# Optimization experiments

Hardware: AMD Instinct MI355X
Metric: run time of the kernel (lower is better)

The kernel has to match this reference:

```python
import jax, jax.numpy as jnp
import numpy as np

B, IN_DIM = 1024, 128
MBD_IN, MBD_OUT, MBD_K = 64, 50, 5
BN_EPS = 1e-5


def setup_inputs() -> dict:
    key = jax.random.key(0)
    ks = jax.random.split(key, 16)
    n = lambda k, s: jax.random.normal(k, s, dtype=jnp.float32)
    return {
        "x": n(ks[0], (B, IN_DIM)),
        # MLP: 128->256->128(BN)->64, LeakyReLU(0.2)
        "W1": n(ks[1], (IN_DIM, 256)) * 0.05, "b1": jnp.zeros((256,), jnp.float32),
        "W2": n(ks[2], (256, 128)) * 0.05, "b2": jnp.zeros((128,), jnp.float32),
        "gamma": jnp.ones((128,), jnp.float32), "beta": jnp.zeros((128,), jnp.float32),
        "W3": n(ks[3], (128, 64)) * 0.05, "b3": jnp.zeros((64,), jnp.float32),
        # SelfAttention1D(64, heads=1) on a length-1 token: softmax over a single
        # key is identically 1, so output = residual + out_proj(value_proj(h)).
        # Wq/Wk provably do not affect the output and are omitted.
        "Wv": n(ks[4], (64, 64)) * 0.05, "bv": jnp.zeros((64,), jnp.float32),
        "Wo": n(ks[5], (64, 64)) * 0.05, "bo": jnp.zeros((64,), jnp.float32),
        # MinibatchDiscrimination tensor T: [64, 50, 5], init 0.05*randn as in source
        "T": n(ks[6], (MBD_IN, MBD_OUT, MBD_K)) * 0.05,
        "Ws": n(ks[7], (MBD_IN + MBD_OUT, 1)) * 0.05, "bs": jnp.zeros((1,), jnp.float32),
    }


def _lrelu(h):
    return jnp.where(h > 0, h, 0.2 * h)


def reference(x, W1, b1, W2, b2, gamma, beta, W3, b3, Wv, bv, Wo, bo, T, Ws, bs):
    # --- MLP backbone (BatchNorm1d in training mode: batch statistics) ---
    h = _lrelu(x @ W1 + b1)                      # [B,256]
    h = h @ W2 + b2                              # [B,128]
    mu = h.mean(axis=0)
    var = ((h - mu) ** 2).mean(axis=0)           # biased variance (torch BN)
    h = (h - mu) * jax.lax.rsqrt(var + BN_EPS) * gamma + beta
    h = _lrelu(h)
    h = _lrelu(h @ W3 + b3)                      # [B,64]
    # --- SelfAttention1D, seq_len=1 -> attn weights == 1 ---
    h = h + (h @ Wv + bv) @ Wo + bo              # [B,64]
    # --- Minibatch discrimination: fused all-pairs L1 + exp-sum ---
    M = (h @ T.reshape(MBD_IN, MBD_OUT * MBD_K)).reshape(-1, MBD_OUT, MBD_K)  # [B,50,5]
    diff = jnp.abs(M[:, None, :, :] - M[None, :, :, :]).sum(-1)               # [B,B,50]
    o = jnp.exp(-diff).sum(axis=0) - 1.0          # [B,50] (self term exp(0)=1 removed)
    feat = jnp.concatenate([h, o], axis=1)        # [B,114]
    score = (feat @ Ws + bs).squeeze(-1)          # [B]
    return score
```

## Files before the change

kernel.cpp:

```cpp
#include <hip/hip_runtime.h>
#include <math.h>

#define LRELU(v) ((v) > 0.f ? (v) : 0.2f * (v))

__global__ __launch_bounds__(256) void k1_mlp12(
    const float* __restrict__ x,
    const float* __restrict__ W1, const float* __restrict__ b1,
    const float* __restrict__ W2, const float* __restrict__ b2,
    float* __restrict__ h2g, float* __restrict__ stats)
{
    __shared__ float xs[256];
    __shared__ float h1s[512];
    __shared__ float ssum[256];
    __shared__ float ssq[256];
    const int t = threadIdx.x;
    const int r0 = blockIdx.x * 2;

    xs[t] = x[r0 * 128 + t];
    __syncthreads();

    {
        float a0 = b1[t], a1 = a0;
        for (int k = 0; k < 128; ++k) {
            float w = W1[k * 256 + t];
            a0 += xs[k] * w;
            a1 += xs[128 + k] * w;
        }
        h1s[t] = LRELU(a0);
        h1s[256 + t] = LRELU(a1);
    }
    __syncthreads();

    {
        const int c = t & 127;
        const int rr = t >> 7;
        float a = b2[c];
        for (int k = 0; k < 256; ++k)
            a += h1s[rr * 256 + k] * W2[k * 128 + c];
        h2g[(r0 + rr) * 128 + c] = a;
        ssum[t] = a;
        ssq[t] = a * a;
    }
    __syncthreads();
    if (t < 128)      atomicAdd(stats + t, ssum[t] + ssum[128 + t]);
    else { int c = t - 128; atomicAdd(stats + 128 + c, ssq[c] + ssq[128 + c]); }
}

__global__ __launch_bounds__(256) void k2_bn_attn_m(
    const float* __restrict__ h2g, const float* __restrict__ stats,
    const float* __restrict__ gamma, const float* __restrict__ beta,
    const float* __restrict__ W3, const float* __restrict__ b3,
    const float* __restrict__ Wv, const float* __restrict__ bv,
    const float* __restrict__ Wo, const float* __restrict__ bo,
    const float* __restrict__ T2,
    float* __restrict__ h4g, float* __restrict__ Mt)
{
    __shared__ float a[256];
    __shared__ float h3s[128];
    __shared__ float vss[128];
    __shared__ float h4s[128];
    const int t = threadIdx.x;
    const int r0 = blockIdx.x * 2;

    {
        const int c = t & 127;
        float s = stats[c], ss = stats[128 + c];
        float mean = s * (1.f / 1024.f);
        float var = ss * (1.f / 1024.f) - mean * mean;
        float rstd = rsqrtf(var + 1e-5f);
        float v = (h2g[r0 * 128 + t] - mean) * rstd * gamma[c] + beta[c];
        a[t] = LRELU(v);
    }
    __syncthreads();

    const int row = t >> 6, col = t & 63;
    if (t < 128) {
        float acc = b3[col];
        for (int k = 0; k < 128; ++k) acc += a[row * 128 + k] * W3[k * 64 + col];
        h3s[row * 64 + col] = LRELU(acc);
    }
    __syncthreads();
    if (t < 128) {
        float acc = bv[col];
        for (int k = 0; k < 64; ++k) acc += h3s[row * 64 + k] * Wv[k * 64 + col];
        vss[row * 64 + col] = acc;
    }
    __syncthreads();
    if (t < 128) {
        float acc = bo[col];
        for (int k = 0; k < 64; ++k) acc += vss[row * 64 + k] * Wo[k * 64 + col];
        float h4 = h3s[row * 64 + col] + acc;
        h4s[row * 64 + col] = h4;
        h4g[(r0 + row) * 64 + col] = h4;
    }
    __syncthreads();

    if (t < 250) {
        float m0 = 0.f, m1 = 0.f;
        for (int k = 0; k < 64; ++k) {
            float w = T2[k * 250 + t];
            m0 += h4s[k] * w;
            m1 += h4s[64 + k] * w;
        }
        Mt[(size_t)t * 1024 + r0]     = m0;
        Mt[(size_t)t * 1024 + r0 + 1] = m1;
    } else {
        Mt[(size_t)t * 1024 + r0]     = 0.f;
        Mt[(size_t)t * 1024 + r0 + 1] = 0.f;
    }
    if (t < 4) {
        Mt[(size_t)(256 + t) * 1024 + r0]     = 0.f;
        Mt[(size_t)(256 + t) * 1024 + r0 + 1] = 0.f;
    }
}

__global__ __launch_bounds__(256) void k3_pairs(
    const float* __restrict__ Mt, float* __restrict__ opart)
{
    __shared__ float mi[2560];
    const int t = threadIdx.x;
    const int b = blockIdx.x;
    const int jt = b / 104;
    const int rem = b - jt * 104;
    const int ct = rem >> 3;
    const int ic = rem & 7;
    const int jl = t & 63, cl = t >> 6;
    const int j = jt * 64 + jl;
    const int c = ct * 4 + cl;
    const int i0 = ic * 128;

    for (int qq = 0; qq < 10; ++qq) {
        int idx = qq * 256 + t;
        int cc = idx >> 7, il = idx & 127;
        mi[idx] = Mt[(size_t)(ct * 20 + cc) * 1024 + i0 + il];
    }

    float mj0 = Mt[(size_t)(c * 5 + 0) * 1024 + j];
    float mj1 = Mt[(size_t)(c * 5 + 1) * 1024 + j];
    float mj2 = Mt[(size_t)(c * 5 + 2) * 1024 + j];
    float mj3 = Mt[(size_t)(c * 5 + 3) * 1024 + j];
    float mj4 = Mt[(size_t)(c * 5 + 4) * 1024 + j];
    __syncthreads();

    const float2* m0 = (const float2*)(mi + (cl * 5 + 0) * 128);
    const float2* m1 = (const float2*)(mi + (cl * 5 + 1) * 128);
    const float2* m2 = (const float2*)(mi + (cl * 5 + 2) * 128);
    const float2* m3 = (const float2*)(mi + (cl * 5 + 3) * 128);
    const float2* m4 = (const float2*)(mi + (cl * 5 + 4) * 128);

    float acc0 = 0.f, acc1 = 0.f;
    for (int p = 0; p < 64; ++p) {
        float2 v0 = m0[p], v1 = m1[p], v2 = m2[p], v3 = m3[p], v4 = m4[p];
        float d0 = fabsf(v0.x - mj0) + fabsf(v1.x - mj1) + fabsf(v2.x - mj2)
                 + fabsf(v3.x - mj3) + fabsf(v4.x - mj4);
        float d1 = fabsf(v0.y - mj0) + fabsf(v1.y - mj1) + fabsf(v2.y - mj2)
                 + fabsf(v3.y - mj3) + fabsf(v4.y - mj4);
        acc0 += __expf(-d0);
        acc1 += __expf(-d1);
    }
    opart[(size_t)(ic * 1024 + j) * 52 + c] = acc0 + acc1;
}

__global__ __launch_bounds__(64) void k4_score(
    const float* __restrict__ h4g, const float* __restrict__ opart,
    const float* __restrict__ Ws, const float* __restrict__ bs,
    float* __restrict__ out)
{
    const int j = blockIdx.x, t = threadIdx.x;
    float contrib = h4g[j * 64 + t] * Ws[t];
    if (t < 50) {
        float s = 0.f;
        for (int ic = 0; ic < 8; ++ic)
            s += opart[(size_t)(ic * 1024 + j) * 52 + t];
        contrib += (s - 1.0f) * Ws[64 + t];
    }
    for (int off = 32; off > 0; off >>= 1)
        contrib += __shfl_down(contrib, off, 64);
    if (t == 0) out[j] = contrib + bs[0];
}

extern "C" void kernel_launch(void* const* d_in, const int* in_sizes, int n_in,
                              void* d_out, int out_size, void* d_ws, size_t ws_size,
                              hipStream_t stream)
{
    const float* x     = (const float*)d_in[0];
    const float* W1    = (const float*)d_in[1];
    const float* b1    = (const float*)d_in[2];
    const float* W2    = (const float*)d_in[3];
    const float* b2    = (const float*)d_in[4];
    const float* gamma = (const float*)d_in[5];
    const float* beta  = (const float*)d_in[6];
    const float* W3    = (const float*)d_in[7];
    const float* b3    = (const float*)d_in[8];
    const float* Wv    = (const float*)d_in[9];
    const float* bv    = (const float*)d_in[10];
    const float* Wo    = (const float*)d_in[11];
    const float* bo    = (const float*)d_in[12];
    const float* T2    = (const float*)d_in[13];
    const float* Ws    = (const float*)d_in[14];
    const float* bs    = (const float*)d_in[15];

    float* ws    = (float*)d_ws;
    float* h2    = ws + 0;
    float* stats = ws + 131072;
    float* h4    = ws + 131328;
    float* Mt    = ws + 196864;
    float* opart = ws + 463104;
    float* out   = (float*)d_out;

    hipMemsetAsync(stats, 0, 256 * sizeof(float), stream);
    hipLaunchKernelGGL(k1_mlp12, dim3(512), dim3(256), 0, stream,
                       x, W1, b1, W2, b2, h2, stats);
    hipLaunchKernelGGL(k2_bn_attn_m, dim3(512), dim3(256), 0, stream,
                       h2, stats, gamma, beta, W3, b3, Wv, bv, Wo, bo, T2, h4, Mt);
    hipLaunchKernelGGL(k3_pairs, dim3(1664), dim3(256), 0, stream, Mt, opart);
    hipLaunchKernelGGL(k4_score, dim3(1024), dim3(64), 0, stream,
                       h4, opart, Ws, bs, out);
}
```

Before: 141.2 us.

## Fuse MLP stages with grid barrier and fold score into last pair block

Merges the first two kernels into one by putting a software grid-wide barrier (atomic counter spin) after the BatchNorm statistics accumulation, so h2 stays in shared memory and no longer goes through global memory. The final score kernel is folded into the pairwise kernel: the last block to finish each j-tile, found with an atomic ticket counter, reduces the partial sums and writes the output. Two kernel launches go away. The spin barrier assumes all 512 blocks are co-resident (launch_bounds min 2 blocks per CU), which risks deadlock if occupancy is insufficient.

Result: slower. 223.2 us (+58.1%).

```diff
diff --git a/kernel.cpp b/kernel.cpp
--- a/kernel.cpp
+++ b/kernel.cpp
@@ -3,22 +3,31 @@
 
 #define LRELU(v) ((v) > 0.f ? (v) : 0.2f * (v))
 
-__global__ __launch_bounds__(256) void k1_mlp12(
+__global__ __launch_bounds__(256, 2) void kA(
     const float* __restrict__ x,
     const float* __restrict__ W1, const float* __restrict__ b1,
     const float* __restrict__ W2, const float* __restrict__ b2,
-    float* __restrict__ h2g, float* __restrict__ stats)
+    const float* __restrict__ gamma, const float* __restrict__ beta,
+    const float* __restrict__ W3, const float* __restrict__ b3,
+    const float* __restrict__ Wv, const float* __restrict__ bv,
+    const float* __restrict__ Wo, const float* __restrict__ bo,
+    const float* __restrict__ T2,
+    float* __restrict__ stats, unsigned int* __restrict__ cnt,
+    float* __restrict__ h4g, float* __restrict__ Mt)
 {
     __shared__ float xs[256];
     __shared__ float h1s[512];
-    __shared__ float ssum[256];
-    __shared__ float ssq[256];
+    __shared__ float h2loc[256];
+    __shared__ float sq[256];
+    __shared__ float a[256];
+    __shared__ float h3s[128];
+    __shared__ float vss[128];
+    __shared__ float h4s[128];
     const int t = threadIdx.x;
     const int r0 = blockIdx.x * 2;
 
     xs[t] = x[r0 * 128 + t];
     __syncthreads();
-
     {
         float a0 = b1[t], a1 = a0;
         for (int k = 0; k < 128; ++k) {
@@ -30,49 +39,40 @@
         h1s[256 + t] = LRELU(a1);
     }
     __syncthreads();
-
     {
         const int c = t & 127;
         const int rr = t >> 7;
-        float a = b2[c];
+        float v = b2[c];
         for (int k = 0; k < 256; ++k)
-            a += h1s[rr * 256 + k] * W2[k * 128 + c];
-        h2g[(r0 + rr) * 128 + c] = a;
-        ssum[t] = a;
-        ssq[t] = a * a;
-    }
-    __syncthreads();
-    if (t < 128)      atomicAdd(stats + t, ssum[t] + ssum[128 + t]);
-    else { int c = t - 128; atomicAdd(stats + 128 + c, ssq[c] + ssq[128 + c]); }
-}
-
-__global__ __launch_bounds__(256) void k2_bn_attn_m(
-    const float* __restrict__ h2g, const float* __restrict__ stats,
-    const float* __restrict__ gamma, const float* __restrict__ beta,
-    const float* __restrict__ W3, const float* __restrict__ b3,
-    const float* __restrict__ Wv, const float* __restrict__ bv,
-    const float* __restrict__ Wo, const float* __restrict__ bo,
-    const float* __restrict__ T2,
-    float* __restrict__ h4g, float* __restrict__ Mt)
-{
-    __shared__ float a[256];
-    __shared__ float h3s[128];
-    __shared__ float vss[128];
-    __shared__ float h4s[128];
-    const int t = threadIdx.x;
-    const int r0 = blockIdx.x * 2;
+            v += h1s[rr * 256 + k] * W2[k * 128 + c];
+        h2loc[t] = v;
+        sq[t] = v * v;
+    }
+    __syncthreads();
+    if (t < 128)      atomicAdd(stats + t, h2loc[t] + h2loc[128 + t]);
+    else { int c = t - 128; atomicAdd(stats + 128 + c, sq[c] + sq[128 + c]); }
+
+    __syncthreads();
+    if (t == 0) {
+        __threadfence();
+        atomicAdd(cnt, 1u);
+        while (__hip_atomic_load(cnt, __ATOMIC_RELAXED, __HIP_MEMORY_SCOPE_AGENT) < 512u)
+            __builtin_amdgcn_s_sleep(2);
+    }
+    __syncthreads();
+    __threadfence();
 
     {
         const int c = t & 127;
-        float s = stats[c], ss = stats[128 + c];
+        float s  = __hip_atomic_load(stats + c,       __ATOMIC_RELAXED, __HIP_MEMORY_SCOPE_AGENT);
+        float ss = __hip_atomic_load(stats + 128 + c, __ATOMIC_RELAXED, __HIP_MEMORY_SCOPE_AGENT);
         float mean = s * (1.f / 1024.f);
         float var = ss * (1.f / 1024.f) - mean * mean;
         float rstd = rsqrtf(var + 1e-5f);
-        float v = (h2g[r0 * 128 + t] - mean) * rstd * gamma[c] + beta[c];
+        float v = (h2loc[t] - mean) * rstd * gamma[c] + beta[c];
         a[t] = LRELU(v);
     }
     __syncthreads();
-
     const int row = t >> 6, col = t & 63;
     if (t < 128) {
         float acc = b3[col];
@@ -94,7 +94,6 @@
         h4g[(r0 + row) * 64 + col] = h4;
     }
     __syncthreads();
-
     if (t < 250) {
         float m0 = 0.f, m1 = 0.f;
         for (int k = 0; k < 64; ++k) {
@@ -114,10 +113,14 @@
     }
 }
 
-__global__ __launch_bounds__(256) void k3_pairs(
-    const float* __restrict__ Mt, float* __restrict__ opart)
+__global__ __launch_bounds__(256) void kB(
+    const float* __restrict__ Mt, float* __restrict__ opart,
+    unsigned int* __restrict__ cnt2,
+    const float* __restrict__ h4g, const float* __restrict__ Ws,
+    const float* __restrict__ bs, float* __restrict__ out)
 {
     __shared__ float mi[2560];
+    __shared__ unsigned int lastflag;
     const int t = threadIdx.x;
     const int b = blockIdx.x;
     const int jt = b / 104;
@@ -134,7 +137,6 @@
         int cc = idx >> 7, il = idx & 127;
         mi[idx] = Mt[(size_t)(ct * 20 + cc) * 1024 + i0 + il];
     }
-
     float mj0 = Mt[(size_t)(c * 5 + 0) * 1024 + j];
     float mj1 = Mt[(size_t)(c * 5 + 1) * 1024 + j];
     float mj2 = Mt[(size_t)(c * 5 + 2) * 1024 + j];
@@ -149,8 +151,8 @@
     const float2* m4 = (const float2*)(mi + (cl * 5 + 4) * 128);
 
     float acc0 = 0.f, acc1 = 0.f;
-    for (int p = 0; p < 64; ++p) {
-        float2 v0 = m0[p], v1 = m1[p], v2 = m2[p], v3 = m3[p], v4 = m4[p];
+    for (int q = 0; q < 64; ++q) {
+        float2 v0 = m0[q], v1 = m1[q], v2 = m2[q], v3 = m3[q], v4 = m4[q];
         float d0 = fabsf(v0.x - mj0) + fabsf(v1.x - mj1) + fabsf(v2.x - mj2)
                  + fabsf(v3.x - mj3) + fabsf(v4.x - mj4);
         float d1 = fabsf(v0.y - mj0) + fabsf(v1.y - mj1) + fabsf(v2.y - mj2)
@@ -158,25 +160,34 @@
         acc0 += __expf(-d0);
         acc1 += __expf(-d1);
     }
-    opart[(size_t)(ic * 1024 + j) * 52 + c] = acc0 + acc1;
-}
-
-__global__ __launch_bounds__(64) void k4_score(
-    const float* __restrict__ h4g, const float* __restrict__ opart,
-    const float* __restrict__ Ws, const float* __restrict__ bs,
-    float* __restrict__ out)
-{
-    const int j = blockIdx.x, t = threadIdx.x;
-    float contrib = h4g[j * 64 + t] * Ws[t];
-    if (t < 50) {
-        float s = 0.f;
-        for (int ic = 0; ic < 8; ++ic)
-            s += opart[(size_t)(ic * 1024 + j) * 52 + t];
-        contrib += (s - 1.0f) * Ws[64 + t];
-    }
-    for (int off = 32; off > 0; off >>= 1)
-        contrib += __shfl_down(contrib, off, 64);
-    if (t == 0) out[j] = contrib + bs[0];
+    __hip_atomic_store(opart + (size_t)(ic * 1024 + j) * 52 + c, acc0 + acc1,
+                       __ATOMIC_RELAXED, __HIP_MEMORY_SCOPE_AGENT);
+
+    __syncthreads();
+    if (t == 0) {
+        __threadfence();
+        lastflag = (atomicAdd(cnt2 + jt, 1u) == 103u) ? 1u : 0u;
+    }
+    __syncthreads();
+    if (lastflag) {
+        __threadfence();
+        const int w = t >> 6, lane = t & 63;
+        for (int ii = 0; ii < 16; ++ii) {
+            const int jj = jt * 64 + w * 16 + ii;
+            float contrib = h4g[jj * 64 + lane] * Ws[lane];
+            if (lane < 50) {
+                float s = 0.f;
+                for (int icc = 0; icc < 8; ++icc)
+                    s += __hip_atomic_load(
+                        opart + (size_t)(icc * 1024 + jj) * 52 + lane,
+                        __ATOMIC_RELAXED, __HIP_MEMORY_SCOPE_AGENT);
+                contrib += (s - 1.0f) * Ws[64 + lane];
+            }
+            for (int off = 32; off > 0; off >>= 1)
+                contrib += __shfl_down(contrib, off, 64);
+            if (lane == 0) out[jj] = contrib + bs[0];
+        }
+    }
 }
 
 extern "C" void kernel_launch(void* const* d_in, const int* in_sizes, int n_in,
@@ -200,20 +211,19 @@
     const float* Ws    = (const float*)d_in[14];
     const float* bs    = (const float*)d_in[15];
 
-    float* ws    = (float*)d_ws;
-    float* h2    = ws + 0;
-    float* stats = ws + 131072;
-    float* h4    = ws + 131328;
-    float* Mt    = ws + 196864;
-    float* opart = ws + 463104;
-    float* out   = (float*)d_out;
-
-    hipMemsetAsync(stats, 0, 256 * sizeof(float), stream);
-    hipLaunchKernelGGL(k1_mlp12, dim3(512), dim3(256), 0, stream,
-                       x, W1, b1, W2, b2, h2, stats);
-    hipLaunchKernelGGL(k2_bn_attn_m, dim3(512), dim3(256), 0, stream,
-                       h2, stats, gamma, beta, W3, b3, Wv, bv, Wo, bo, T2, h4, Mt);
-    hipLaunchKernelGGL(k3_pairs, dim3(1664), dim3(256), 0, stream, Mt, opart);
-    hipLaunchKernelGGL(k4_score, dim3(1024), dim3(64), 0, stream,
-                       h4, opart, Ws, bs, out);
+    float* ws = (float*)d_ws;
+    float* stats        = ws + 0;
+    unsigned int* cnts  = (unsigned int*)(ws + 256);
+    float* h4           = ws + 512;
+    float* Mt           = ws + 66048;
+    float* opart        = ws + 332288;
+    float* out          = (float*)d_out;
+
+    hipMemsetAsync(ws, 0, 2048, stream);
+
+    hipLaunchKernelGGL(kA, dim3(512), dim3(256), 0, stream,
+                       x, W1, b1, W2, b2, gamma, beta, W3, b3,
+                       Wv, bv, Wo, bo, T2, stats, cnts, h4, Mt);
+    hipLaunchKernelGGL(kB, dim3(1664), dim3(256), 0, stream,
+                       Mt, opart, cnts + 1, h4, Ws, bs, out);
 }
```
